# Kernel tuning notes

Measured on AMD Instinct MI355X. Metric: run time of the kernel, lower is better.

Reference implementation:

```python
import jax, jax.numpy as jnp
import numpy as np

GROUPS = 8
EPS = 1e-5


def setup_inputs() -> dict:
    key = jax.random.key(0)
    ks = jax.random.split(key, 6)
    b, c, h, w = 4, 256, 64, 64
    x = jax.random.normal(ks[0], (b, c, h, w), dtype=jnp.float32)
    norm_w = jnp.ones((c,), jnp.float32)
    norm_b = jnp.zeros((c,), jnp.float32)
    # 1x1 convs == channel matmuls; store weights as [out, in]
    qkv_w = jax.random.normal(ks[1], (3 * c, c), jnp.float32) / np.sqrt(c)
    qkv_b = jax.random.normal(ks[2], (3 * c,), jnp.float32) * 0.01
    out_w = jax.random.normal(ks[3], (c, c), jnp.float32) / np.sqrt(c)
    out_b = jax.random.normal(ks[4], (c,), jnp.float32) * 0.01
    return {"x": x, "norm_w": norm_w, "norm_b": norm_b,
            "qkv_w": qkv_w, "qkv_b": qkv_b, "out_w": out_w, "out_b": out_b}


def group_norm(x, weight, bias):
    b, c, h, w = x.shape
    xg = x.reshape(b, GROUPS, c // GROUPS, h, w)
    mean = xg.mean(axis=(2, 3, 4), keepdims=True)
    var = xg.var(axis=(2, 3, 4), keepdims=True)
    xg = (xg - mean) * jax.lax.rsqrt(var + EPS)
    x = xg.reshape(b, c, h, w)
    return x * weight[None, :, None, None] + bias[None, :, None, None]


def reference(x, norm_w, norm_b, qkv_w, qkv_b, out_w, out_b):
    b, c, h, w = x.shape
    n = h * w
    hn = group_norm(x, norm_w, norm_b).reshape(b, c, n)  # [b,c,n]
    qkv = jnp.einsum('oc,bcn->bon', qkv_w, hn) + qkv_b[None, :, None]
    q, k, v = qkv[:, :c], qkv[:, c:2 * c], qkv[:, 2 * c:]
    scale = c ** (-0.5)
    attn = jnp.einsum('bci,bcj->bij', q, k) * scale  # [b,n,n]
    attn = jax.nn.softmax(attn, axis=-1)
    o = jnp.einsum('bcj,bij->bci', v, attn)  # [b,c,n]
    o = jnp.einsum('oc,bcn->bon', out_w, o) + out_b[None, :, None]
    return x + o.reshape(b, c, h, w)
```

## Files before the change

### kernel.cpp

```cpp
#include <hip/hip_runtime.h>

typedef __bf16 bf16x8 __attribute__((ext_vector_type(8)));
typedef float  f32x4  __attribute__((ext_vector_type(4)));
typedef float  f32x16 __attribute__((ext_vector_type(16)));
typedef unsigned int   u32x4 __attribute__((ext_vector_type(4)));
typedef unsigned short u16x4 __attribute__((ext_vector_type(4)));

#define NB   4
#define NC   256
#define NN   4096
#define NO   768
#define NPG  131072
#define KVB  32

#define AS1 __attribute__((address_space(1)))
#define AS3 __attribute__((address_space(3)))

__device__ __forceinline__ unsigned short f2b(float f){
  unsigned int u = __builtin_bit_cast(unsigned int, f);
  u += 0x7fff + ((u >> 16) & 1);
  return (unsigned short)(u >> 16);
}
__device__ __forceinline__ float b2f(unsigned short s){
  unsigned int u = (unsigned int)s << 16;
  return __builtin_bit_cast(float, u);
}

#define SWZ(e, r) ((e) ^ (((r) & 7) << 3))

__global__ void gn_stats(const float* __restrict__ x, float* __restrict__ part){
  const f32x4* p = (const f32x4*)x + (size_t)blockIdx.x * 4096;
  float s = 0.f, ss = 0.f;
  for (int i = threadIdx.x; i < 4096; i += 256){
    f32x4 v = p[i];
    s  += v[0] + v[1] + v[2] + v[3];
    ss += v[0]*v[0] + v[1]*v[1] + v[2]*v[2] + v[3]*v[3];
  }
  #pragma unroll
  for (int o = 32; o; o >>= 1){ s += __shfl_down(s, o); ss += __shfl_down(ss, o); }
  __shared__ float red[8];
  int wid = threadIdx.x >> 6;
  if ((threadIdx.x & 63) == 0){ red[wid] = s; red[wid + 4] = ss; }
  __syncthreads();
  if (threadIdx.x == 0){
    part[blockIdx.x*2]     = red[0] + red[1] + red[2] + red[3];
    part[blockIdx.x*2 + 1] = red[4] + red[5] + red[6] + red[7];
  }
}

__global__ void gn_apply(const float* __restrict__ x, const float* __restrict__ part,
                         const float* __restrict__ nw, const float* __restrict__ nb,
                         unsigned short* __restrict__ hn){
  size_t i4 = (size_t)blockIdx.x * 256 + threadIdx.x;
  int bg = (int)(i4 >> 15);
  int c  = (int)((i4 >> 10) & 255);
  float s = 0.f, ss = 0.f;
  #pragma unroll
  for (int p2 = 0; p2 < 8; ++p2){
    s  += part[(bg*8 + p2)*2];
    ss += part[(bg*8 + p2)*2 + 1];
  }
  float mean = s * (1.f / NPG);
  float var  = ss * (1.f / NPG) - mean * mean;
  float rstd = rsqrtf(var + 1e-5f);
  float w  = nw[c] * rstd;
  float bb = nb[c] - mean * w;
  f32x4 v = ((const f32x4*)x)[i4];
  u16x4 o4;
  o4[0] = f2b(v[0]*w + bb); o4[1] = f2b(v[1]*w + bb);
  o4[2] = f2b(v[2]*w + bb); o4[3] = f2b(v[3]*w + bb);
  ((u16x4*)hn)[i4] = o4;
}

__global__ __launch_bounds__(256) void qkv_gemm(
    const unsigned short* __restrict__ hn, const float* __restrict__ W,
    const float* __restrict__ bias, unsigned short* __restrict__ qsep,
    unsigned short* __restrict__ ksep, unsigned short* __restrict__ vsep){
  __shared__ __align__(16) unsigned short a_lds[128*32];
  __shared__ __align__(16) unsigned short b_lds[128*32];
  const int n0 = blockIdx.x * 128, o0 = blockIdx.y * 128, b = blockIdx.z;
  const unsigned short* hb = hn + (size_t)b * NC * NN;
  const int t = threadIdx.x, lane = t & 63, wid = t >> 6;
  const int wm = wid >> 1, wn = wid & 1;
  const int l15 = lane & 15, lk = (lane >> 4) * 8;
  f32x4 acc[4][4] = {};
  for (int k0 = 0; k0 < NC; k0 += 32){
    __syncthreads();
    for (int ch = t; ch < 512; ch += 256){
      int row = ch >> 2, kc = (ch & 3) * 8;
      const float* src = W + (size_t)(o0 + row) * NC + k0 + kc;
      unsigned short tmp[8];
      #pragma unroll
      for (int e = 0; e < 8; ++e) tmp[e] = f2b(src[e]);
      *(u32x4*)&a_lds[SWZ(row*32 + kc, row)] = *(u32x4*)tmp;
    }
    for (int ch = t; ch < 512; ch += 256){
      int kk = ch >> 4, j8 = (ch & 15) * 8;
      const unsigned short* src = hb + (size_t)(k0 + kk) * NN + n0 + j8;
      unsigned short tmp[8];
      *(u32x4*)tmp = *(const u32x4*)src;
      #pragma unroll
      for (int e = 0; e < 8; ++e) b_lds[SWZ((j8+e)*32 + kk, j8+e)] = tmp[e];
    }
    __syncthreads();
    bf16x8 af[4], bfr[4];
    #pragma unroll
    for (int mf = 0; mf < 4; ++mf){
      int r = wm*64 + mf*16 + l15;
      af[mf] = __builtin_bit_cast(bf16x8, *(u32x4*)&a_lds[SWZ(r*32 + lk, r)]);
    }
    #pragma unroll
    for (int nf = 0; nf < 4; ++nf){
      int r = wn*64 + nf*16 + l15;
      bfr[nf] = __builtin_bit_cast(bf16x8, *(u32x4*)&b_lds[SWZ(r*32 + lk, r)]);
    }
    #pragma unroll
    for (int mf = 0; mf < 4; ++mf)
      #pragma unroll
      for (int nf = 0; nf < 4; ++nf)
        acc[mf][nf] = __builtin_amdgcn_mfma_f32_16x16x32_bf16(af[mf], bfr[nf], acc[mf][nf], 0, 0, 0);
  }
  size_t nb_ = (size_t)b * NN * NC;
  unsigned short* vs = vsep + (size_t)b * NC * NN;
  #pragma unroll
  for (int mf = 0; mf < 4; ++mf){
    int ob = o0 + wm*64 + mf*16 + ((lane >> 4) << 2);
    float b0 = bias[ob], b1 = bias[ob+1], b2 = bias[ob+2], b3 = bias[ob+3];
    #pragma unroll
    for (int nf = 0; nf < 4; ++nf){
      int n = n0 + wn*64 + nf*16 + l15;
      f32x4 a = acc[mf][nf];
      u16x4 stv;
      stv[0] = f2b(a[0] + b0); stv[1] = f2b(a[1] + b1);
      stv[2] = f2b(a[2] + b2); stv[3] = f2b(a[3] + b3);
      if (ob < 256){
        *(u16x4*)(qsep + nb_ + (size_t)n * NC + ob) = stv;
      } else if (ob < 512){
        *(u16x4*)(ksep + nb_ + (size_t)n * NC + (ob - 256)) = stv;
      } else {
        vs[(size_t)(ob - 512 + 0) * NN + n] = stv[0];
        vs[(size_t)(ob - 512 + 1) * NN + n] = stv[1];
        vs[(size_t)(ob - 512 + 2) * NN + n] = stv[2];
        vs[(size_t)(ob - 512 + 3) * NN + n] = stv[3];
      }
    }
  }
}

__global__ __launch_bounds__(256, 2) void attn(
    const unsigned short* __restrict__ qsep,
    const unsigned short* __restrict__ ksep,
    const unsigned short* __restrict__ vsep,
    unsigned short* __restrict__ opart, float* __restrict__ ml){
  __shared__ __align__(16) unsigned short k_lds[2][KVB*256];
  __shared__ __align__(16) unsigned short v_lds[2][256*KVB];
  const int swzb = (blockIdx.x & 7) * 64 + (blockIdx.x >> 3);
  const int part = swzb >> 7;
  const int b    = (swzb >> 5) & 3;
  const int i0   = (swzb & 31) * 128;
  const int jbase = part * 1024;
  const unsigned short* qb_ = qsep + (size_t)b * NN * NC;
  const unsigned short* kb_ = ksep + (size_t)b * NN * NC;
  const unsigned short* vb_ = vsep + (size_t)b * NC * NN;
  const int t = threadIdx.x, lane = t & 63, wid = t >> 6;
  const int l31 = lane & 31, hi = lane >> 5;

  bf16x8 qf[16];
  {
    const unsigned short* qrow = qb_ + (size_t)(i0 + wid*32 + l31) * NC + hi*8;
    #pragma unroll
    for (int ks = 0; ks < 16; ++ks)
      qf[ks] = __builtin_bit_cast(bf16x8, *(const u32x4*)&qrow[ks*16]);
  }

  int koff[4], voff[4];
  #pragma unroll
  for (int q = 0; q < 4; ++q){
    int jr = (wid*4 + q)*2 + (lane >> 5);
    int cc = (lane & 31) ^ (jr & 7);
    koff[q] = jr*256 + cc*8;
    int c  = (wid*4 + q)*16 + (lane >> 2);
    int jj = (lane & 3) ^ ((lane >> 2) & 3);
    voff[q] = c*4096 + jj*8;
  }

  auto stage = [&](int buf, int j0) __attribute__((always_inline)) {
    #pragma unroll
    for (int q = 0; q < 4; ++q)
      __builtin_amdgcn_global_load_lds(
          (AS1 const unsigned int*)(kb_ + j0*256 + koff[q]),
          (AS3 unsigned int*)&k_lds[buf][(wid*4 + q)*512], 16, 0, 0);
    #pragma unroll
    for (int q = 0; q < 4; ++q)
      __builtin_amdgcn_global_load_lds(
          (AS1 const unsigned int*)(vb_ + voff[q] + j0),
          (AS3 unsigned int*)&v_lds[buf][(wid*4 + q)*512], 16, 0, 0);
  };

  f32x16 oa[8] = {};
  float m_run = -3.0e38f, l_run = 0.f;

  stage(0, jbase);
  for (int jt = 0; jt < 32; ++jt){
    const int cur = jt & 1;
    if (jt < 31){
      stage(cur ^ 1, jbase + (jt + 1) * KVB);
      asm volatile("s_waitcnt vmcnt(8)" ::: "memory");
    } else {
      asm volatile("s_waitcnt vmcnt(0)" ::: "memory");
    }
    __builtin_amdgcn_sched_barrier(0);
    __builtin_amdgcn_s_barrier();
    __builtin_amdgcn_sched_barrier(0);

    const unsigned short* kl = k_lds[cur];
    const unsigned short* vl = v_lds[cur];
    f32x16 st = {};
    #pragma unroll
    for (int ks = 0; ks < 16; ++ks){
      int e = l31*256 + ks*16 + hi*8;
      bf16x8 ka = __builtin_bit_cast(bf16x8, *(const u32x4*)&kl[SWZ(e, l31)]);
      st = __builtin_amdgcn_mfma_f32_32x32x16_bf16(ka, qf[ks], st, 0, 0, 0);
    }
    float mx = st[0];
    #pragma unroll
    for (int r = 1; r < 16; ++r) mx = fmaxf(mx, st[r]);
    mx *= 0.0625f;
    mx = fmaxf(mx, __shfl_xor(mx, 32));
    if (!__all(mx <= m_run + 8.f)){
      float mnew  = fmaxf(m_run, mx);
      float alpha = __expf(m_run - mnew);
      m_run = mnew; l_run *= alpha;
      #pragma unroll
      for (int tt = 0; tt < 8; ++tt) oa[tt] *= alpha;
    }
    float p[16], lsum = 0.f;
    #pragma unroll
    for (int r = 0; r < 16; ++r){ p[r] = __expf(st[r]*0.0625f - m_run); lsum += p[r]; }
    l_run += lsum + __shfl_xor(lsum, 32);
    unsigned int w[8];
    #pragma unroll
    for (int r = 0; r < 8; ++r){
      unsigned int pk;
      asm("v_cvt_pk_bf16_f32 %0, %1, %2" : "=v"(pk) : "v"(p[2*r]), "v"(p[2*r+1]));
      w[r] = pk;
    }
    asm("v_permlane32_swap_b32 %0, %1" : "+v"(w[0]), "+v"(w[2]));
    asm("v_permlane32_swap_b32 %0, %1" : "+v"(w[1]), "+v"(w[3]));
    asm("v_permlane32_swap_b32 %0, %1" : "+v"(w[4]), "+v"(w[6]));
    asm("v_permlane32_swap_b32 %0, %1" : "+v"(w[5]), "+v"(w[7]));
    u32x4 pb0v = {w[0], w[1], w[2], w[3]};
    u32x4 pb1v = {w[4], w[5], w[6], w[7]};
    bf16x8 pb0 = __builtin_bit_cast(bf16x8, pb0v);
    bf16x8 pb1 = __builtin_bit_cast(bf16x8, pb1v);
    #pragma unroll
    for (int ct = 0; ct < 8; ++ct){
      int c = ct*32 + l31;
      int e0 = c*KVB + hi*8;
      bf16x8 va0 = __builtin_bit_cast(bf16x8, *(const u32x4*)&vl[e0 ^ ((c & 3) << 3)]);
      oa[ct] = __builtin_amdgcn_mfma_f32_32x32x16_bf16(va0, pb0, oa[ct], 0, 0, 0);
      bf16x8 va1 = __builtin_bit_cast(bf16x8, *(const u32x4*)&vl[(e0 + 16) ^ ((c & 3) << 3)]);
      oa[ct] = __builtin_amdgcn_mfma_f32_32x32x16_bf16(va1, pb1, oa[ct], 0, 0, 0);
    }
    __builtin_amdgcn_sched_barrier(0);
    __builtin_amdgcn_s_barrier();
    __builtin_amdgcn_sched_barrier(0);
  }

  size_t orow = ((size_t)(part*4 + b) * NN + i0 + wid*32 + l31) * NC;
  #pragma unroll
  for (int ct = 0; ct < 8; ++ct){
    #pragma unroll
    for (int rq = 0; rq < 4; ++rq){
      unsigned int lo, hi2;
      asm("v_cvt_pk_bf16_f32 %0, %1, %2" : "=v"(lo)  : "v"(oa[ct][4*rq+0]), "v"(oa[ct][4*rq+1]));
      asm("v_cvt_pk_bf16_f32 %0, %1, %2" : "=v"(hi2) : "v"(oa[ct][4*rq+2]), "v"(oa[ct][4*rq+3]));
      int c = ct*32 + rq*8 + 4*hi;
      uint2 pkv; pkv.x = lo; pkv.y = hi2;
      *(uint2*)(opart + orow + c) = pkv;
    }
  }
  if (lane < 32){
    float2 mlv; mlv.x = m_run; mlv.y = l_run;
    ((float2*)ml)[(size_t)(part*4 + b) * NN + i0 + wid*32 + lane] = mlv;
  }
}

__global__ __launch_bounds__(256) void attn_merge(
    const unsigned short* __restrict__ opart, const float* __restrict__ ml,
    unsigned short* __restrict__ ot){
  const int t = threadIdx.x;
  const int row = blockIdx.x * 8 + (t >> 5);
  const int c0 = (t & 31) * 8;
  const float2* mlp = (const float2*)ml;
  float2 m0 = mlp[row], m1 = mlp[16384 + row], m2 = mlp[32768 + row], m3 = mlp[49152 + row];
  float M = fmaxf(fmaxf(m0.x, m1.x), fmaxf(m2.x, m3.x));
  float w0 = __expf(m0.x - M), w1 = __expf(m1.x - M);
  float w2 = __expf(m2.x - M), w3 = __expf(m3.x - M);
  float inv = 1.f / (w0*m0.y + w1*m1.y + w2*m2.y + w3*m3.y);
  w0 *= inv; w1 *= inv; w2 *= inv; w3 *= inv;
  const size_t base = (size_t)row * NC + c0;
  const size_t ps = (size_t)16384 * NC;
  u16x4 a0 = *(const u16x4*)(opart + base),        a1 = *(const u16x4*)(opart + base + 4);
  u16x4 b0 = *(const u16x4*)(opart + base + ps),   b1 = *(const u16x4*)(opart + base + ps + 4);
  u16x4 c0v = *(const u16x4*)(opart + base + 2*ps), c1 = *(const u16x4*)(opart + base + 2*ps + 4);
  u16x4 d0 = *(const u16x4*)(opart + base + 3*ps), d1 = *(const u16x4*)(opart + base + 3*ps + 4);
  u16x4 o0, o1;
  #pragma unroll
  for (int k = 0; k < 4; ++k){
    o0[k] = f2b(w0*b2f(a0[k]) + w1*b2f(b0[k]) + w2*b2f(c0v[k]) + w3*b2f(d0[k]));
    o1[k] = f2b(w0*b2f(a1[k]) + w1*b2f(b1[k]) + w2*b2f(c1[k]) + w3*b2f(d1[k]));
  }
  unsigned short* dst = ot + base;
  *(u16x4*)dst = o0; *(u16x4*)(dst + 4) = o1;
}

__global__ __launch_bounds__(256) void out_proj(
    const unsigned short* __restrict__ ot, const float* __restrict__ W,
    const float* __restrict__ bias, const float* __restrict__ x,
    float* __restrict__ out){
  __shared__ __align__(16) unsigned short a_lds[128*32];
  __shared__ __align__(16) unsigned short b_lds[128*32];
  const int n0 = blockIdx.x * 128, oc0 = blockIdx.y * 128, b = blockIdx.z;
  const unsigned short* ob_ = ot + (size_t)b * NN * NC;
  const int t = threadIdx.x, lane = t & 63, wid = t >> 6;
  const int wm = wid >> 1, wn = wid & 1;
  const int l15 = lane & 15, lk = (lane >> 4) * 8;
  f32x4 acc[4][4] = {};
  for (int k0 = 0; k0 < NC; k0 += 32){
    __syncthreads();
    for (int ch = t; ch < 512; ch += 256){
      int row = ch >> 2, kc = (ch & 3) * 8;
      *(u32x4*)&a_lds[SWZ(row*32 + kc, row)] =
          *(const u32x4*)&ob_[(size_t)(n0 + row) * NC + k0 + kc];
    }
    for (int ch = t; ch < 512; ch += 256){
      int row = ch >> 2, kc = (ch & 3) * 8;
      const float* src = W + (size_t)(oc0 + row) * NC + k0 + kc;
      unsigned short tmp[8];
      #pragma unroll
      for (int e = 0; e < 8; ++e) tmp[e] = f2b(src[e]);
      *(u32x4*)&b_lds[SWZ(row*32 + kc, row)] = *(u32x4*)tmp;
    }
    __syncthreads();
    bf16x8 af[4], bfr[4];
    #pragma unroll
    for (int mf = 0; mf < 4; ++mf){
      int r = wm*64 + mf*16 + l15;
      af[mf] = __builtin_bit_cast(bf16x8, *(u32x4*)&a_lds[SWZ(r*32 + lk, r)]);
    }
    #pragma unroll
    for (int nf = 0; nf < 4; ++nf){
      int r = wn*64 + nf*16 + l15;
      bfr[nf] = __builtin_bit_cast(bf16x8, *(u32x4*)&b_lds[SWZ(r*32 + lk, r)]);
    }
    #pragma unroll
    for (int mf = 0; mf < 4; ++mf)
      #pragma unroll
      for (int nf = 0; nf < 4; ++nf)
        acc[mf][nf] = __builtin_amdgcn_mfma_f32_16x16x32_bf16(af[mf], bfr[nf], acc[mf][nf], 0, 0, 0);
  }
  #pragma unroll
  for (int nf = 0; nf < 4; ++nf){
    int oc = oc0 + wn*64 + nf*16 + l15;
    float bb = bias[oc];
    #pragma unroll
    for (int mf = 0; mf < 4; ++mf){
      int n = n0 + wm*64 + mf*16 + ((lane >> 4) << 2);
      size_t off = ((size_t)b * NC + oc) * NN + n;
      f32x4 xv = *(const f32x4*)&x[off];
      f32x4 r = acc[mf][nf] + xv + bb;
      *(f32x4*)&out[off] = r;
    }
  }
}

extern "C" void kernel_launch(void* const* d_in, const int* in_sizes, int n_in,
                              void* d_out, int out_size, void* d_ws, size_t ws_size,
                              hipStream_t stream){
  const float* x    = (const float*)d_in[0];
  const float* nw   = (const float*)d_in[1];
  const float* nbv  = (const float*)d_in[2];
  const float* qkvw = (const float*)d_in[3];
  const float* qkvb = (const float*)d_in[4];
  const float* outw = (const float*)d_in[5];
  const float* outb = (const float*)d_in[6];
  float* out = (float*)d_out;
  char* ws = (char*)d_ws;
  float*          part  = (float*)ws;
  unsigned short* opart = (unsigned short*)(ws + 4096);
  unsigned short* hn    = (unsigned short*)(ws + 4096);
  unsigned short* qsep  = (unsigned short*)(ws + 4096 + 33554432);
  unsigned short* ksep  = qsep + (size_t)NB*NN*NC;
  unsigned short* vsep  = ksep + (size_t)NB*NN*NC;
  float*          ml    = (float*)(vsep + (size_t)NB*NN*NC);
  unsigned short* ot    = qsep;

  gn_stats<<<256, 256, 0, stream>>>(x, part);
  gn_apply<<<4096, 256, 0, stream>>>(x, part, nw, nbv, hn);
  qkv_gemm<<<dim3(32, 6, 4), 256, 0, stream>>>(hn, qkvw, qkvb, qsep, ksep, vsep);
  attn<<<dim3(512), 256, 0, stream>>>(qsep, ksep, vsep, opart, ml);
  attn_merge<<<dim3(2048), 256, 0, stream>>>(opart, ml, ot);
  out_proj<<<dim3(32, 2, 4), 256, 0, stream>>>(ot, outw, outb, x, out);
}
```

Baseline: 182.0 us.

## Fold softmax scale into Q, split QK accumulators, widen V swizzle, add setprio

Moves the 1/16 softmax scale into the QKV projection epilogue so the attention loop no longer multiplies scores. It splits the QK^T MFMA chain into two independent accumulators to shorten the dependency chain, and uses tree reductions for the row max and sum. It changes the V LDS swizzle from 4-way to 8-way XOR, with a matching permuted global_load_lds source mapping, to reduce bank conflicts. It also raises wave priority around the MFMA blocks. Scaling Q before bf16 rounding shifts rounding slightly, and the new swizzle mapping must stay consistent between the writes and the reads.

Measured after the change: 239.2 us. 1.31x slower.

```diff
diff --git a/kernel.cpp b/kernel.cpp
--- a/kernel.cpp
+++ b/kernel.cpp
@@ -131,13 +131,17 @@
       int n = n0 + wn*64 + nf*16 + l15;
       f32x4 a = acc[mf][nf];
       u16x4 stv;
-      stv[0] = f2b(a[0] + b0); stv[1] = f2b(a[1] + b1);
-      stv[2] = f2b(a[2] + b2); stv[3] = f2b(a[3] + b3);
       if (ob < 256){
+        stv[0] = f2b((a[0] + b0)*0.0625f); stv[1] = f2b((a[1] + b1)*0.0625f);
+        stv[2] = f2b((a[2] + b2)*0.0625f); stv[3] = f2b((a[3] + b3)*0.0625f);
         *(u16x4*)(qsep + nb_ + (size_t)n * NC + ob) = stv;
       } else if (ob < 512){
+        stv[0] = f2b(a[0] + b0); stv[1] = f2b(a[1] + b1);
+        stv[2] = f2b(a[2] + b2); stv[3] = f2b(a[3] + b3);
         *(u16x4*)(ksep + nb_ + (size_t)n * NC + (ob - 256)) = stv;
       } else {
+        stv[0] = f2b(a[0] + b0); stv[1] = f2b(a[1] + b1);
+        stv[2] = f2b(a[2] + b2); stv[3] = f2b(a[3] + b3);
         vs[(size_t)(ob - 512 + 0) * NN + n] = stv[0];
         vs[(size_t)(ob - 512 + 1) * NN + n] = stv[1];
         vs[(size_t)(ob - 512 + 2) * NN + n] = stv[2];
@@ -179,9 +183,11 @@
     int jr = (wid*4 + q)*2 + (lane >> 5);
     int cc = (lane & 31) ^ (jr & 7);
     koff[q] = jr*256 + cc*8;
-    int c  = (wid*4 + q)*16 + (lane >> 2);
-    int jj = (lane & 3) ^ ((lane >> 2) & 3);
-    voff[q] = c*4096 + jj*8;
+    int p = (wid*4 + q)*64 + lane;
+    int l = (p & ~7) | ((((p>>2)^(p>>4))&1)<<2)
+                     | ((((p>>1)^(p>>3))&1)<<1)
+                     | ((p ^ (p>>2) ^ (p>>4)) & 1);
+    voff[q] = (l >> 2)*NN + (l & 3)*8;
   }
 
   auto stage = [&](int buf, int j0) __attribute__((always_inline)) {
@@ -215,18 +221,27 @@
 
     const unsigned short* kl = k_lds[cur];
     const unsigned short* vl = v_lds[cur];
-    f32x16 st = {};
-    #pragma unroll
-    for (int ks = 0; ks < 16; ++ks){
-      int e = l31*256 + ks*16 + hi*8;
-      bf16x8 ka = __builtin_bit_cast(bf16x8, *(const u32x4*)&kl[SWZ(e, l31)]);
-      st = __builtin_amdgcn_mfma_f32_32x32x16_bf16(ka, qf[ks], st, 0, 0, 0);
-    }
-    float mx = st[0];
-    #pragma unroll
-    for (int r = 1; r < 16; ++r) mx = fmaxf(mx, st[r]);
-    mx *= 0.0625f;
-    mx = fmaxf(mx, __shfl_xor(mx, 32));
+    f32x16 sa = {}, sb = {};
+    __builtin_amdgcn_s_setprio(1);
+    #pragma unroll
+    for (int ks = 0; ks < 8; ++ks){
+      int ea = l31*256 + (2*ks)*16 + hi*8;
+      bf16x8 ka = __builtin_bit_cast(bf16x8, *(const u32x4*)&kl[SWZ(ea, l31)]);
+      sa = __builtin_amdgcn_mfma_f32_32x32x16_bf16(ka, qf[2*ks], sa, 0, 0, 0);
+      int eb = l31*256 + (2*ks+1)*16 + hi*8;
+      bf16x8 kb2 = __builtin_bit_cast(bf16x8, *(const u32x4*)&kl[SWZ(eb, l31)]);
+      sb = __builtin_amdgcn_mfma_f32_32x32x16_bf16(kb2, qf[2*ks+1], sb, 0, 0, 0);
+    }
+    __builtin_amdgcn_s_setprio(0);
+    f32x16 st = sa + sb;
+    float m8[8];
+    #pragma unroll
+    for (int i = 0; i < 8; ++i) m8[i] = fmaxf(st[i], st[i+8]);
+    #pragma unroll
+    for (int o = 4; o; o >>= 1)
+      #pragma unroll
+      for (int i = 0; i < 4; ++i) if (i < o) m8[i] = fmaxf(m8[i], m8[i+o]);
+    float mx = fmaxf(m8[0], __shfl_xor(m8[0], 32));
     if (!__all(mx <= m_run + 8.f)){
       float mnew  = fmaxf(m_run, mx);
       float alpha = __expf(m_run - mnew);
@@ -234,10 +249,17 @@
       #pragma unroll
       for (int tt = 0; tt < 8; ++tt) oa[tt] *= alpha;
     }
-    float p[16], lsum = 0.f;
-    #pragma unroll
-    for (int r = 0; r < 16; ++r){ p[r] = __expf(st[r]*0.0625f - m_run); lsum += p[r]; }
-    l_run += lsum + __shfl_xor(lsum, 32);
+    float p[16];
+    #pragma unroll
+    for (int r = 0; r < 16; ++r) p[r] = __expf(st[r] - m_run);
+    float s8[8];
+    #pragma unroll
+    for (int i = 0; i < 8; ++i) s8[i] = p[i] + p[i+8];
+    #pragma unroll
+    for (int o = 4; o; o >>= 1)
+      #pragma unroll
+      for (int i = 0; i < 4; ++i) if (i < o) s8[i] += s8[i+o];
+    l_run += s8[0] + __shfl_xor(s8[0], 32);
     unsigned int w[8];
     #pragma unroll
     for (int r = 0; r < 8; ++r){
@@ -253,15 +275,17 @@
     u32x4 pb1v = {w[4], w[5], w[6], w[7]};
     bf16x8 pb0 = __builtin_bit_cast(bf16x8, pb0v);
     bf16x8 pb1 = __builtin_bit_cast(bf16x8, pb1v);
+    __builtin_amdgcn_s_setprio(1);
     #pragma unroll
     for (int ct = 0; ct < 8; ++ct){
       int c = ct*32 + l31;
-      int e0 = c*KVB + hi*8;
-      bf16x8 va0 = __builtin_bit_cast(bf16x8, *(const u32x4*)&vl[e0 ^ ((c & 3) << 3)]);
+      int sw = (c & 7) << 3;
+      bf16x8 va0 = __builtin_bit_cast(bf16x8, *(const u32x4*)&vl[(c*KVB + hi*8) ^ sw]);
       oa[ct] = __builtin_amdgcn_mfma_f32_32x32x16_bf16(va0, pb0, oa[ct], 0, 0, 0);
-      bf16x8 va1 = __builtin_bit_cast(bf16x8, *(const u32x4*)&vl[(e0 + 16) ^ ((c & 3) << 3)]);
+      bf16x8 va1 = __builtin_bit_cast(bf16x8, *(const u32x4*)&vl[(c*KVB + hi*8 + 16) ^ sw]);
       oa[ct] = __builtin_amdgcn_mfma_f32_32x32x16_bf16(va1, pb1, oa[ct], 0, 0, 0);
     }
+    __builtin_amdgcn_s_setprio(0);
     __builtin_amdgcn_sched_barrier(0);
     __builtin_amdgcn_s_barrier();
     __builtin_amdgcn_sched_barrier(0);
```

## Software-pipeline PV matmul one tile behind QK and pre-scale Q

Applied to the files above, without the earlier changes.

Restructures the attention loop so the PV MFMAs for the previous KV tile are issued right after the current tile's QK MFMAs, with the softmax moved to the end of the iteration. The intent is to let the exp and packing work overlap with matrix-core work instead of serialising behind it. This needs a third V LDS buffer, which raises shared memory use and may lower occupancy at two blocks per CU. Separately, Q is multiplied by the softmax scale of 0.0625 in the QKV projection epilogue, which removes the per-element scale multiply inside the attention loop.

New measurement: 203.0 us. 1.12x slower.

```diff
diff --git a/kernel.cpp b/kernel.cpp
--- a/kernel.cpp
+++ b/kernel.cpp
@@ -131,13 +131,17 @@
       int n = n0 + wn*64 + nf*16 + l15;
       f32x4 a = acc[mf][nf];
       u16x4 stv;
-      stv[0] = f2b(a[0] + b0); stv[1] = f2b(a[1] + b1);
-      stv[2] = f2b(a[2] + b2); stv[3] = f2b(a[3] + b3);
       if (ob < 256){
+        stv[0] = f2b((a[0] + b0)*0.0625f); stv[1] = f2b((a[1] + b1)*0.0625f);
+        stv[2] = f2b((a[2] + b2)*0.0625f); stv[3] = f2b((a[3] + b3)*0.0625f);
         *(u16x4*)(qsep + nb_ + (size_t)n * NC + ob) = stv;
       } else if (ob < 512){
+        stv[0] = f2b(a[0] + b0); stv[1] = f2b(a[1] + b1);
+        stv[2] = f2b(a[2] + b2); stv[3] = f2b(a[3] + b3);
         *(u16x4*)(ksep + nb_ + (size_t)n * NC + (ob - 256)) = stv;
       } else {
+        stv[0] = f2b(a[0] + b0); stv[1] = f2b(a[1] + b1);
+        stv[2] = f2b(a[2] + b2); stv[3] = f2b(a[3] + b3);
         vs[(size_t)(ob - 512 + 0) * NN + n] = stv[0];
         vs[(size_t)(ob - 512 + 1) * NN + n] = stv[1];
         vs[(size_t)(ob - 512 + 2) * NN + n] = stv[2];
@@ -153,7 +157,7 @@
     const unsigned short* __restrict__ vsep,
     unsigned short* __restrict__ opart, float* __restrict__ ml){
   __shared__ __align__(16) unsigned short k_lds[2][KVB*256];
-  __shared__ __align__(16) unsigned short v_lds[2][256*KVB];
+  __shared__ __align__(16) unsigned short v_lds[3][256*KVB];
   const int swzb = (blockIdx.x & 7) * 64 + (blockIdx.x >> 3);
   const int part = swzb >> 7;
   const int b    = (swzb >> 5) & 3;
@@ -184,37 +188,24 @@
     voff[q] = c*4096 + jj*8;
   }
 
-  auto stage = [&](int buf, int j0) __attribute__((always_inline)) {
+  auto stage = [&](int kbuf, int vbuf, int j0) __attribute__((always_inline)) {
     #pragma unroll
     for (int q = 0; q < 4; ++q)
       __builtin_amdgcn_global_load_lds(
           (AS1 const unsigned int*)(kb_ + j0*256 + koff[q]),
-          (AS3 unsigned int*)&k_lds[buf][(wid*4 + q)*512], 16, 0, 0);
+          (AS3 unsigned int*)&k_lds[kbuf][(wid*4 + q)*512], 16, 0, 0);
     #pragma unroll
     for (int q = 0; q < 4; ++q)
       __builtin_amdgcn_global_load_lds(
           (AS1 const unsigned int*)(vb_ + voff[q] + j0),
-          (AS3 unsigned int*)&v_lds[buf][(wid*4 + q)*512], 16, 0, 0);
+          (AS3 unsigned int*)&v_lds[vbuf][(wid*4 + q)*512], 16, 0, 0);
   };
 
   f32x16 oa[8] = {};
   float m_run = -3.0e38f, l_run = 0.f;
-
-  stage(0, jbase);
-  for (int jt = 0; jt < 32; ++jt){
-    const int cur = jt & 1;
-    if (jt < 31){
-      stage(cur ^ 1, jbase + (jt + 1) * KVB);
-      asm volatile("s_waitcnt vmcnt(8)" ::: "memory");
-    } else {
-      asm volatile("s_waitcnt vmcnt(0)" ::: "memory");
-    }
-    __builtin_amdgcn_sched_barrier(0);
-    __builtin_amdgcn_s_barrier();
-    __builtin_amdgcn_sched_barrier(0);
-
-    const unsigned short* kl = k_lds[cur];
-    const unsigned short* vl = v_lds[cur];
+  bf16x8 pb0 = {}, pb1 = {};
+
+  auto qk = [&](const unsigned short* kl) __attribute__((always_inline)) {
     f32x16 st = {};
     #pragma unroll
     for (int ks = 0; ks < 16; ++ks){
@@ -222,37 +213,9 @@
       bf16x8 ka = __builtin_bit_cast(bf16x8, *(const u32x4*)&kl[SWZ(e, l31)]);
       st = __builtin_amdgcn_mfma_f32_32x32x16_bf16(ka, qf[ks], st, 0, 0, 0);
     }
-    float mx = st[0];
-    #pragma unroll
-    for (int r = 1; r < 16; ++r) mx = fmaxf(mx, st[r]);
-    mx *= 0.0625f;
-    mx = fmaxf(mx, __shfl_xor(mx, 32));
-    if (!__all(mx <= m_run + 8.f)){
-      float mnew  = fmaxf(m_run, mx);
-      float alpha = __expf(m_run - mnew);
-      m_run = mnew; l_run *= alpha;
-      #pragma unroll
-      for (int tt = 0; tt < 8; ++tt) oa[tt] *= alpha;
-    }
-    float p[16], lsum = 0.f;
-    #pragma unroll
-    for (int r = 0; r < 16; ++r){ p[r] = __expf(st[r]*0.0625f - m_run); lsum += p[r]; }
-    l_run += lsum + __shfl_xor(lsum, 32);
-    unsigned int w[8];
-    #pragma unroll
-    for (int r = 0; r < 8; ++r){
-      unsigned int pk;
-      asm("v_cvt_pk_bf16_f32 %0, %1, %2" : "=v"(pk) : "v"(p[2*r]), "v"(p[2*r+1]));
-      w[r] = pk;
-    }
-    asm("v_permlane32_swap_b32 %0, %1" : "+v"(w[0]), "+v"(w[2]));
-    asm("v_permlane32_swap_b32 %0, %1" : "+v"(w[1]), "+v"(w[3]));
-    asm("v_permlane32_swap_b32 %0, %1" : "+v"(w[4]), "+v"(w[6]));
-    asm("v_permlane32_swap_b32 %0, %1" : "+v"(w[5]), "+v"(w[7]));
-    u32x4 pb0v = {w[0], w[1], w[2], w[3]};
-    u32x4 pb1v = {w[4], w[5], w[6], w[7]};
-    bf16x8 pb0 = __builtin_bit_cast(bf16x8, pb0v);
-    bf16x8 pb1 = __builtin_bit_cast(bf16x8, pb1v);
+    return st;
+  };
+  auto pv = [&](const unsigned short* vl) __attribute__((always_inline)) {
     #pragma unroll
     for (int ct = 0; ct < 8; ++ct){
       int c = ct*32 + l31;
@@ -262,10 +225,60 @@
       bf16x8 va1 = __builtin_bit_cast(bf16x8, *(const u32x4*)&vl[(e0 + 16) ^ ((c & 3) << 3)]);
       oa[ct] = __builtin_amdgcn_mfma_f32_32x32x16_bf16(va1, pb1, oa[ct], 0, 0, 0);
     }
+  };
+  auto smx = [&](f32x16 st) __attribute__((always_inline)) {
+    float mx = st[0];
+    #pragma unroll
+    for (int r = 1; r < 16; ++r) mx = fmaxf(mx, st[r]);
+    mx = fmaxf(mx, __shfl_xor(mx, 32));
+    if (!__all(mx <= m_run + 8.f)){
+      float mnew  = fmaxf(m_run, mx);
+      float alpha = __expf(m_run - mnew);
+      m_run = mnew; l_run *= alpha;
+      #pragma unroll
+      for (int tt = 0; tt < 8; ++tt) oa[tt] *= alpha;
+    }
+    float p[16], lsum = 0.f;
+    #pragma unroll
+    for (int r = 0; r < 16; ++r){ p[r] = __expf(st[r] - m_run); lsum += p[r]; }
+    l_run += lsum + __shfl_xor(lsum, 32);
+    unsigned int w[8];
+    #pragma unroll
+    for (int r = 0; r < 8; ++r){
+      unsigned int pk;
+      asm("v_cvt_pk_bf16_f32 %0, %1, %2" : "=v"(pk) : "v"(p[2*r]), "v"(p[2*r+1]));
+      w[r] = pk;
+    }
+    asm("v_permlane32_swap_b32 %0, %1" : "+v"(w[0]), "+v"(w[2]));
+    asm("v_permlane32_swap_b32 %0, %1" : "+v"(w[1]), "+v"(w[3]));
+    asm("v_permlane32_swap_b32 %0, %1" : "+v"(w[4]), "+v"(w[6]));
+    asm("v_permlane32_swap_b32 %0, %1" : "+v"(w[5]), "+v"(w[7]));
+    u32x4 pb0v = {w[0], w[1], w[2], w[3]};
+    u32x4 pb1v = {w[4], w[5], w[6], w[7]};
+    pb0 = __builtin_bit_cast(bf16x8, pb0v);
+    pb1 = __builtin_bit_cast(bf16x8, pb1v);
+  };
+
+  stage(0, 0, jbase);
+  for (int jt = 0; jt < 32; ++jt){
+    const int cur = jt & 1;
+    if (jt < 31){
+      stage(cur ^ 1, (jt + 1) % 3, jbase + (jt + 1) * KVB);
+      asm volatile("s_waitcnt vmcnt(8)" ::: "memory");
+    } else {
+      asm volatile("s_waitcnt vmcnt(0)" ::: "memory");
+    }
     __builtin_amdgcn_sched_barrier(0);
     __builtin_amdgcn_s_barrier();
     __builtin_amdgcn_sched_barrier(0);
-  }
+    f32x16 st = qk(k_lds[cur]);
+    if (jt > 0) pv(v_lds[(jt - 1) % 3]);
+    __builtin_amdgcn_sched_barrier(0);
+    __builtin_amdgcn_s_barrier();
+    __builtin_amdgcn_sched_barrier(0);
+    smx(st);
+  }
+  pv(v_lds[31 % 3]);
 
   size_t orow = ((size_t)(part*4 + b) * NN + i0 + wid*32 + l31) * NC;
   #pragma unroll
```
